# Kernel tuning notes

Hardware: AMD Instinct MI355X
Metric: run time of the kernel (lower is better)

Reference implementation:

```python
import jax, jax.numpy as jnp
import numpy as np

# ---- hash-grid constants (from tcnn Encoding config in __init__) ----
N_LEVELS = 16
F = 2                      # n_features_per_level
LOG2_T = 19
T = 1 << LOG2_T            # hashmap entries per level
BASE_RES = 16
PER_LEVEL_SCALE = 1.447269237440378
PRIMES = np.array([1, 2654435761, 805459861], dtype=np.uint32)
# corner offsets of the unit cube, shape [8, 3]
OFFS = np.stack(np.meshgrid([0, 1], [0, 1], [0, 1], indexing='ij'), -1).reshape(8, 3)


def hash_grid_encode(x01, table):
    """x01: [N,3] in [0,1]; table: [L, T, F]. Returns [N, L*F]."""
    offs = jnp.asarray(OFFS, dtype=jnp.int32)          # [8,3]
    primes = jnp.asarray(PRIMES)                       # [3] uint32
    feats = []
    for l in range(N_LEVELS):
        scale = BASE_RES * (PER_LEVEL_SCALE ** l) - 1.0   # tcnn grid scale
        res = int(np.ceil(scale)) + 1                      # grid resolution
        pos = x01 * scale + 0.5                            # [N,3]
        pos0 = jnp.floor(pos)
        w = pos - pos0                                     # trilinear fracs [N,3]
        pos0 = pos0.astype(jnp.int32)
        corners = jnp.clip(pos0[:, None, :] + offs[None], 0, res - 1)  # [N,8,3]
        if res ** 3 <= T:
            # dense (stride) indexing fits in the table
            idx = (corners[..., 0]
                   + res * corners[..., 1]
                   + res * res * corners[..., 2]).astype(jnp.int32)    # [N,8]
        else:
            # spatial hash with uint32 wraparound multiply + xor
            cu = corners.astype(jnp.uint32)
            idx = ((cu[..., 0] * primes[0])
                   ^ (cu[..., 1] * primes[1])
                   ^ (cu[..., 2] * primes[2])) & jnp.uint32(T - 1)
            idx = idx.astype(jnp.int32)
        # trilinear weights: prod over dims of (w if offset==1 else 1-w)
        wc = jnp.where(offs[None].astype(bool), w[:, None, :], 1.0 - w[:, None, :])
        wc = wc.prod(-1)                                   # [N,8]
        g = table[l][idx]                                  # gather -> [N,8,F]
        feats.append(jnp.einsum('nc,ncf->nf', wc, g))      # [N,F]
    return jnp.concatenate(feats, -1)                      # [N, L*F]


def mlp2(x, w1, w2):
    # 2-layer bias-free MLP with ReLU, matching MLP(num_layers=2, bias=False)
    return jnp.maximum(x @ w1, 0.0) @ w2


def setup_inputs() -> dict:
    key = jax.random.key(0)
    ks = jax.random.split(key, 6)
    N = 1048576
    points = jax.random.uniform(ks[0], (N, 3), jnp.float32, -1.0, 1.0)  # in bbox [-1,1]^3
    # tcnn hash-grid init: uniform(-1e-4, 1e-4)
    hash_table = jax.random.uniform(ks[1], (N_LEVELS, T, F), jnp.float32, -1e-4, 1e-4)
    enc_dim = N_LEVELS * F  # 32
    dw1 = jax.random.normal(ks[2], (enc_dim, 64), jnp.float32) * (1.0 / np.sqrt(enc_dim))
    dw2 = jax.random.normal(ks[3], (64, 1), jnp.float32) * (1.0 / 8.0)
    fw1 = jax.random.normal(ks[4], (enc_dim, 64), jnp.float32) * (1.0 / np.sqrt(enc_dim))
    fw2 = jax.random.normal(ks[5], (64, 3), jnp.float32) * (1.0 / 8.0)
    return {"points": points, "hash_table": hash_table,
            "dw1": dw1, "dw2": dw2, "fw1": fw1, "fw2": fw2}


def reference(points, hash_table, dw1, dw2, fw1, fw2):
    # contract_to_unisphere with bbox [[-1,-1,-1],[1,1,1]] -> [0,1]^3, clamped
    x01 = jnp.clip((points + 1.0) * 0.5, 0.0, 1.0)
    enc = hash_grid_encode(x01, hash_table)               # [N, 32]
    density = jax.nn.softplus(mlp2(enc, dw1, dw2))        # [N, 1]
    color = jax.nn.sigmoid(mlp2(enc, fw1, fw2))           # [N, 3]
    return color, density
```

## Files before the change

### kernel.cpp

```cpp
#include <hip/hip_runtime.h>
#include <hip/hip_bf16.h>
#include <cmath>

#define NLV 16
#define TBL_SIZE (1u << 19)

#define SORT_PPB 8192
#define SORT_THREADS 512
#define SORT_NKEYS 4096

struct LevelConsts {
    float scale[NLV];
    int   res[NLV];
    int   dense[NLV];
};

__device__ __forceinline__ unsigned int f32_to_bf16_rne(float f) {
    unsigned int u = __float_as_uint(f);
    return (u + 0x7FFFu + ((u >> 16) & 1u)) >> 16;
}
__device__ __forceinline__ unsigned int pack_bf16(float a, float b) {
    return f32_to_bf16_rne(a) | (f32_to_bf16_rne(b) << 16);
}
__device__ __forceinline__ short f32_to_bf16_s(float f) {
    return (short)f32_to_bf16_rne(f);
}
__device__ __forceinline__ float bf16lo_to_f32(unsigned int g) {
    return __uint_as_float(g << 16);
}
__device__ __forceinline__ float bf16hi_to_f32(unsigned int g) {
    return __uint_as_float(g & 0xFFFF0000u);
}

typedef __attribute__((ext_vector_type(8))) short bf16x8;
typedef __attribute__((ext_vector_type(4))) float f32x4;
typedef __attribute__((ext_vector_type(2))) unsigned int u32x2;
typedef __attribute__((ext_vector_type(4))) unsigned int u32x4;

__device__ __forceinline__ unsigned spread3(unsigned x) {
    x &= 0x3FFu;
    x = (x | (x << 16)) & 0x030000FFu;
    x = (x | (x << 8))  & 0x0300F00Fu;
    x = (x | (x << 4))  & 0x030C30C3u;
    x = (x | (x << 2))  & 0x09249249u;
    return x;
}
__device__ __forceinline__ unsigned key12(float px, float py, float pz) {
    float x = fminf(fmaxf((px + 1.0f) * 0.5f, 0.0f), 1.0f);
    float y = fminf(fmaxf((py + 1.0f) * 0.5f, 0.0f), 1.0f);
    float z = fminf(fmaxf((pz + 1.0f) * 0.5f, 0.0f), 1.0f);
    int ix = min((int)(x * 16.0f), 15);
    int iy = min((int)(y * 16.0f), 15);
    int iz = min((int)(z * 16.0f), 15);
    return spread3((unsigned)ix) | (spread3((unsigned)iy) << 1) | (spread3((unsigned)iz) << 2);
}

__global__ __launch_bounds__(SORT_THREADS) void cvt_and_sort(
    const float* __restrict__ tablef32, unsigned int* __restrict__ tbl_out, int npairs,
    const float* __restrict__ pts, f32x4* __restrict__ spts4, int N, int sortBlocks)
{
    __shared__ unsigned hist[SORT_NKEYS];
    __shared__ unsigned wsum[SORT_THREADS / 64];

    if ((int)blockIdx.x < sortBlocks) {
        const int sb   = blockIdx.x;
        const int base = sb * SORT_PPB;
        const int cnt  = min(SORT_PPB, N - base);
        const int tid  = threadIdx.x;
        const int lane = tid & 63, wid = tid >> 6;

        for (int i = tid; i < SORT_NKEYS; i += SORT_THREADS) hist[i] = 0u;
        __syncthreads();

        unsigned short keys[16];
#pragma unroll
        for (int q = 0; q < 16; q++) {
            int idx = q * SORT_THREADS + tid;
            unsigned k = 0xFFFFu;
            if (idx < cnt) {
                int p = base + idx;
                float px = pts[3 * p + 0];
                float py = pts[3 * p + 1];
                float pz = pts[3 * p + 2];
                k = key12(px, py, pz);
                atomicAdd(&hist[k], 1u);
            }
            keys[q] = (unsigned short)k;
        }
        __syncthreads();

        unsigned loc[8], s = 0;
#pragma unroll
        for (int j = 0; j < 8; j++) { loc[j] = hist[tid * 8 + j]; s += loc[j]; }
        unsigned x = s;
#pragma unroll
        for (int d = 1; d < 64; d <<= 1) {
            unsigned y = __shfl_up(x, d, 64);
            if (lane >= d) x += y;
        }
        unsigned wex = x - s;
        if (lane == 63) wsum[wid] = x;
        __syncthreads();
        if (tid == 0) {
            unsigned r = 0;
            for (int i = 0; i < SORT_THREADS / 64; i++) { unsigned t = wsum[i]; wsum[i] = r; r += t; }
        }
        __syncthreads();
        unsigned run = wex + wsum[wid];
#pragma unroll
        for (int j = 0; j < 8; j++) { hist[tid * 8 + j] = run; run += loc[j]; }
        __syncthreads();

#pragma unroll
        for (int q = 0; q < 16; q++) {
            int idx = q * SORT_THREADS + tid;
            if (idx < cnt) {
                int p = base + idx;
                float px = pts[3 * p + 0];
                float py = pts[3 * p + 1];
                float pz = pts[3 * p + 2];
                unsigned pos = atomicAdd(&hist[keys[q]], 1u);
                f32x4 o;
                o.x = px; o.y = py; o.z = pz; o.w = __uint_as_float((unsigned)p);
                spts4[base + pos] = o;
            }
        }
    } else {
        int b = blockIdx.x - sortBlocks;
        int n2 = npairs >> 1;
        int i = b * SORT_THREADS + threadIdx.x;
        int stride = ((int)gridDim.x - sortBlocks) * SORT_THREADS;
        const f32x4* in4 = (const f32x4*)tablef32;
        u32x2* out2 = (u32x2*)tbl_out;
        for (; i < n2; i += stride) {
            f32x4 v = __builtin_nontemporal_load(&in4[i]);
            u32x2 o;
            o.x = pack_bf16(v.x, v.y);
            o.y = pack_bf16(v.z, v.w);
            __builtin_nontemporal_store(o, &out2[i]);
        }
    }
}

__global__ __launch_bounds__(256) void cvt_table(const float* __restrict__ in,
                                                 unsigned int* __restrict__ out, int npairs) {
    int n2 = npairs >> 1;
    int i = blockIdx.x * 256 + threadIdx.x;
    int stride = gridDim.x * 256;
    const f32x4* in4 = (const f32x4*)in;
    u32x2* out2 = (u32x2*)out;
    for (; i < n2; i += stride) {
        f32x4 v = __builtin_nontemporal_load(&in4[i]);
        u32x2 o;
        o.x = pack_bf16(v.x, v.y);
        o.y = pack_bf16(v.z, v.w);
        __builtin_nontemporal_store(o, &out2[i]);
    }
}

#define ENC_P 4
template<int PSTRIDE>
__global__ __launch_bounds__(256) void encode_lvl(
    const float* __restrict__ points,
    const unsigned int* __restrict__ tbl,
    unsigned int* __restrict__ enc,
    int N, LevelConsts C)
{
    const int level = blockIdx.y;
    const float sc    = C.scale[level];
    const int   res   = C.res[level];
    const int   dense = C.dense[level];
    const unsigned int* __restrict__ t = tbl + (size_t)level * TBL_SIZE;
    unsigned int* __restrict__ eo = enc + (size_t)level * N;

    const int base = blockIdx.x * (256 * ENC_P) + threadIdx.x;

    int   pt[ENC_P];
    int   valid[ENC_P];
    float wx[ENC_P], wy[ENC_P], wz[ENC_P];
    unsigned int i0a[ENC_P][4], i1a[ENC_P][4];

#pragma unroll
    for (int q = 0; q < ENC_P; q++) {
        pt[q] = base + q * 256;
        valid[q] = pt[q] < N;
        int p = valid[q] ? pt[q] : 0;
        float px, py, pz;
        if (PSTRIDE == 4) {
            f32x4 v = *(const f32x4*)&points[(size_t)p * 4];
            px = v.x; py = v.y; pz = v.z;
        } else {
            px = points[p * 3 + 0];
            py = points[p * 3 + 1];
            pz = points[p * 3 + 2];
        }
        float x = fminf(fmaxf((px + 1.0f) * 0.5f, 0.0f), 1.0f);
        float y = fminf(fmaxf((py + 1.0f) * 0.5f, 0.0f), 1.0f);
        float z = fminf(fmaxf((pz + 1.0f) * 0.5f, 0.0f), 1.0f);

        float fx = x * sc + 0.5f;
        float fy = y * sc + 0.5f;
        float fz = z * sc + 0.5f;
        float f0x = floorf(fx), f0y = floorf(fy), f0z = floorf(fz);
        wx[q] = fx - f0x; wy[q] = fy - f0y; wz[q] = fz - f0z;
        int ix0 = min(max((int)f0x, 0), res - 1);
        int iy0 = min(max((int)f0y, 0), res - 1);
        int iz0 = min(max((int)f0z, 0), res - 1);
        int ix1 = min(ix0 + 1, res - 1);
        int iy1 = min(iy0 + 1, res - 1);
        int iz1 = min(iz0 + 1, res - 1);

#pragma unroll
        for (int m = 0; m < 4; m++) {
            unsigned int uy = (unsigned int)((m & 1) ? iy1 : iy0);
            unsigned int uz = (unsigned int)((m & 2) ? iz1 : iz0);
            unsigned int i0, i1;
            if (dense) {
                unsigned int b = (unsigned int)res * uy + (unsigned int)(res * res) * uz;
                i0 = (unsigned int)ix0 + b;
                i1 = (unsigned int)ix1 + b;
            } else {
                unsigned int H = uy * 2654435761u ^ uz * 805459861u;
                i0 = ((unsigned int)ix0 ^ H) & (TBL_SIZE - 1u);
                i1 = ((unsigned int)ix1 ^ H) & (TBL_SIZE - 1u);
            }
            i0a[q][m] = i0;
            i1a[q][m] = i1;
        }
    }

    u32x2 pr[ENC_P][4];
#pragma unroll
    for (int q = 0; q < ENC_P; q++)
#pragma unroll
        for (int m = 0; m < 4; m++)
            pr[q][m] = *(const u32x2*)(t + (i0a[q][m] & ~1u));

    unsigned int ex[ENC_P][4];
#pragma unroll
    for (int q = 0; q < ENC_P; q++)
#pragma unroll
        for (int m = 0; m < 4; m++) {
            unsigned int i0 = i0a[q][m], i1 = i1a[q][m];
            unsigned int e = 0u;
            if (i1 != (i0 ^ 1u)) e = t[i1];
            ex[q][m] = e;
        }

#pragma unroll
    for (int q = 0; q < ENC_P; q++) {
        float e0 = 0.0f, e1 = 0.0f;
        float wxq = wx[q];
#pragma unroll
        for (int m = 0; m < 4; m++) {
            unsigned int i0 = i0a[q][m], i1 = i1a[q][m];
            u32x2 P = pr[q][m];
            unsigned int v0   = (i0 & 1u) ? P.y : P.x;
            unsigned int vpar = (i0 & 1u) ? P.x : P.y;
            unsigned int v1   = (i1 == (i0 ^ 1u)) ? vpar : ex[q][m];
            float wyz = (((m & 1) ? wy[q] : 1.0f - wy[q])) *
                        (((m & 2) ? wz[q] : 1.0f - wz[q]));
            float w0 = wyz * (1.0f - wxq);
            float w1 = wyz * wxq;
            e0 = fmaf(w0, bf16lo_to_f32(v0), e0);
            e0 = fmaf(w1, bf16lo_to_f32(v1), e0);
            e1 = fmaf(w0, bf16hi_to_f32(v0), e1);
            e1 = fmaf(w1, bf16hi_to_f32(v1), e1);
        }
        if (valid[q]) __builtin_nontemporal_store(pack_bf16(e0, e1), &eo[pt[q]]);
    }
}

__global__ __launch_bounds__(256, 4) void mlp_kernel(
    const unsigned int* __restrict__ enc,
    const float* __restrict__ dw1, const float* __restrict__ dw2,
    const float* __restrict__ fw1, const float* __restrict__ fw2,
    const unsigned int* __restrict__ perm,
    float* __restrict__ out, int N, int ntiles)
{
    __shared__ unsigned int hsh[4][16][68];
    __shared__ float sOut[4][256];

    const int tid  = threadIdx.x;
    const int wave = tid >> 6;
    const int lane = tid & 63;
    const int l15 = lane & 15;
    const int quad = lane >> 4;

    bf16x8 B1[8];
#pragma unroll
    for (int nt = 0; nt < 8; nt++) {
        int col = nt * 16 + l15;
        const float* w = (col < 64) ? (dw1 + col) : (fw1 + (col - 64));
#pragma unroll
        for (int j = 0; j < 8; j++) {
            int k = quad * 8 + j;
            B1[nt][j] = f32_to_bf16_s(w[k * 64]);
        }
    }

    bf16x8 B2[4];
#pragma unroll
    for (int s = 0; s < 4; s++) {
#pragma unroll
        for (int j = 0; j < 8; j++) {
            int k_lds = s * 32 + quad * 8 + j;
            int hu = ((k_lds & 7) << 4) | (k_lds >> 3);
            float v = 0.0f;
            if (l15 == 0)      v = (hu < 64)  ? dw2[hu] : 0.0f;
            else if (l15 < 4)  v = (hu >= 64) ? fw2[(hu - 64) * 3 + (l15 - 1)] : 0.0f;
            B2[s][j] = f32_to_bf16_s(v);
        }
    }

    for (int tile = blockIdx.x; tile < ntiles; tile += gridDim.x) {
        const int wbase = tile * 256 + wave * 64;

        unsigned int au[4][4];
#pragma unroll
        for (int sub = 0; sub < 4; sub++) {
            int ptc = min(wbase + sub * 16 + l15, N - 1);
#pragma unroll
            for (int j = 0; j < 4; j++)
                au[sub][j] = enc[(size_t)(quad * 4 + j) * N + ptc];
        }

#pragma unroll
        for (int sub = 0; sub < 4; sub++) {
            union { unsigned int u[4]; bf16x8 v; } acvt;
#pragma unroll
            for (int j = 0; j < 4; j++) acvt.u[j] = au[sub][j];

            f32x4 acc1[8];
#pragma unroll
            for (int nt = 0; nt < 8; nt++) {
                acc1[nt] = (f32x4){0.0f, 0.0f, 0.0f, 0.0f};
                acc1[nt] = __builtin_amdgcn_mfma_f32_16x16x32_bf16(acvt.v, B1[nt], acc1[nt], 0, 0, 0);
            }

#pragma unroll
            for (int r = 0; r < 4; r++) {
                u32x4 pk;
#pragma unroll
                for (int d = 0; d < 4; d++) {
                    float h0 = fmaxf(acc1[2 * d + 0][r], 0.0f);
                    float h1 = fmaxf(acc1[2 * d + 1][r], 0.0f);
                    pk[d] = pack_bf16(h0, h1);
                }
                *(u32x4*)&hsh[wave][quad * 4 + r][l15 * 4] = pk;
            }

            f32x4 p0 = (f32x4){0,0,0,0}, p1 = (f32x4){0,0,0,0};
            f32x4 p2 = (f32x4){0,0,0,0}, p3 = (f32x4){0,0,0,0};
            {
                bf16x8 a0 = *(const bf16x8*)&hsh[wave][l15][0 * 16 + quad * 4];
                bf16x8 a1 = *(const bf16x8*)&hsh[wave][l15][1 * 16 + quad * 4];
                bf16x8 a2 = *(const bf16x8*)&hsh[wave][l15][2 * 16 + quad * 4];
                bf16x8 a3 = *(const bf16x8*)&hsh[wave][l15][3 * 16 + quad * 4];
                p0 = __builtin_amdgcn_mfma_f32_16x16x32_bf16(a0, B2[0], p0, 0, 0, 0);
                p1 = __builtin_amdgcn_mfma_f32_16x16x32_bf16(a1, B2[1], p1, 0, 0, 0);
                p2 = __builtin_amdgcn_mfma_f32_16x16x32_bf16(a2, B2[2], p2, 0, 0, 0);
                p3 = __builtin_amdgcn_mfma_f32_16x16x32_bf16(a3, B2[3], p3, 0, 0, 0);
            }
            f32x4 acc2;
#pragma unroll
            for (int r = 0; r < 4; r++) acc2[r] = (p0[r] + p1[r]) + (p2[r] + p3[r]);

            if (l15 < 4) {
#pragma unroll
                for (int r = 0; r < 4; r++)
                    sOut[wave][(sub * 16 + quad * 4 + r) * 4 + l15] = acc2[r];
            }
        }

        if (perm) {
            int p = wbase + lane;
            if (p < N) {
                unsigned int o = perm[(size_t)p * 4 + 3];
                f32x4 v = *(const f32x4*)&sOut[wave][lane * 4];
                float d = v[0];
                d = (d > 20.0f) ? d : log1pf(expf(d));
                out[(size_t)3 * N + o] = d;
                float r0 = 1.0f / (1.0f + expf(-v[1]));
                float g0 = 1.0f / (1.0f + expf(-v[2]));
                float b0 = 1.0f / (1.0f + expf(-v[3]));
                out[(size_t)o * 3 + 0] = r0;
                out[(size_t)o * 3 + 1] = g0;
                out[(size_t)o * 3 + 2] = b0;
            }
        } else {
            long long cmax = ((long long)N - wbase) * 3;
#pragma unroll
            for (int round = 0; round < 3; round++) {
                int f = round * 64 + lane;
                int lp = f / 3, c = f - lp * 3;
                float v = sOut[wave][lp * 4 + 1 + c];
                v = 1.0f / (1.0f + expf(-v));
                if (f < cmax) out[(size_t)wbase * 3 + f] = v;
            }
            {
                int p = wbase + lane;
                float v = sOut[wave][lane * 4];
                v = (v > 20.0f) ? v : log1pf(expf(v));
                if (p < N) out[(size_t)3 * N + p] = v;
            }
        }
    }
}

__global__ __launch_bounds__(256) void nerf_fused(
    const float* __restrict__ points,
    const float* __restrict__ table,
    const float* __restrict__ dw1, const float* __restrict__ dw2,
    const float* __restrict__ fw1, const float* __restrict__ fw2,
    float* __restrict__ out, int N, LevelConsts C)
{
    __shared__ float sD[64 * 32];
    __shared__ float sF[64 * 32];
    __shared__ float sDw2[64];
    __shared__ float sFw2[64 * 3];

    for (int idx = threadIdx.x; idx < 2048; idx += 256) {
        int i = idx >> 6;
        int j = idx & 63;
        sD[j * 32 + i] = dw1[idx];
        sF[j * 32 + i] = fw1[idx];
    }
    if (threadIdx.x < 64)  sDw2[threadIdx.x] = dw2[threadIdx.x];
    if (threadIdx.x < 192) sFw2[threadIdx.x] = fw2[threadIdx.x];
    __syncthreads();

    int gid = blockIdx.x * 256 + threadIdx.x;
    if (gid >= N) return;

    float px = points[gid * 3 + 0];
    float py = points[gid * 3 + 1];
    float pz = points[gid * 3 + 2];
    float x = fminf(fmaxf((px + 1.0f) * 0.5f, 0.0f), 1.0f);
    float y = fminf(fmaxf((py + 1.0f) * 0.5f, 0.0f), 1.0f);
    float z = fminf(fmaxf((pz + 1.0f) * 0.5f, 0.0f), 1.0f);

    float enc[32];

#pragma unroll
    for (int l = 0; l < NLV; l++) {
        const float sc = C.scale[l];
        const int   res = C.res[l];
        const int   dense = C.dense[l];
        const float* __restrict__ tbl = table + (size_t)l * TBL_SIZE * 2;

        float fx = x * sc + 0.5f;
        float fy = y * sc + 0.5f;
        float fz = z * sc + 0.5f;
        float f0x = floorf(fx), f0y = floorf(fy), f0z = floorf(fz);
        float wx = fx - f0x, wy = fy - f0y, wz = fz - f0z;
        int ix0 = min(max((int)f0x, 0), res - 1);
        int iy0 = min(max((int)f0y, 0), res - 1);
        int iz0 = min(max((int)f0z, 0), res - 1);
        int ix1 = min(ix0 + 1, res - 1);
        int iy1 = min(iy0 + 1, res - 1);
        int iz1 = min(iz0 + 1, res - 1);

        float e0 = 0.0f, e1 = 0.0f;
#pragma unroll
        for (int c = 0; c < 8; c++) {
            int cx = (c & 4) ? ix1 : ix0;
            int cy = (c & 2) ? iy1 : iy0;
            int cz = (c & 1) ? iz1 : iz0;
            float wgt = (((c & 4) ? wx : 1.0f - wx) *
                         ((c & 2) ? wy : 1.0f - wy)) *
                         ((c & 1) ? wz : 1.0f - wz);
            unsigned int idx;
            if (dense) {
                idx = (unsigned int)(cx + res * cy + res * res * cz);
            } else {
                idx = ((unsigned int)cx * 1u
                     ^ (unsigned int)cy * 2654435761u
                     ^ (unsigned int)cz * 805459861u) & (TBL_SIZE - 1u);
            }
            const float2 g = *(const float2*)(tbl + (size_t)idx * 2);
            e0 = fmaf(wgt, g.x, e0);
            e1 = fmaf(wgt, g.y, e1);
        }
        enc[2 * l + 0] = e0;
        enc[2 * l + 1] = e1;
    }

    float dacc = 0.0f, c0 = 0.0f, c1 = 0.0f, c2 = 0.0f;
    for (int j = 0; j < 64; j++) {
        float hd = 0.0f, hf = 0.0f;
        const float* __restrict__ colD = &sD[j * 32];
        const float* __restrict__ colF = &sF[j * 32];
#pragma unroll
        for (int i = 0; i < 32; i++) {
            hd = fmaf(enc[i], colD[i], hd);
            hf = fmaf(enc[i], colF[i], hf);
        }
        hd = fmaxf(hd, 0.0f);
        hf = fmaxf(hf, 0.0f);
        dacc = fmaf(hd, sDw2[j], dacc);
        c0 = fmaf(hf, sFw2[j * 3 + 0], c0);
        c1 = fmaf(hf, sFw2[j * 3 + 1], c1);
        c2 = fmaf(hf, sFw2[j * 3 + 2], c2);
    }

    float density = (dacc > 20.0f) ? dacc : log1pf(expf(dacc));
    out[gid * 3 + 0] = 1.0f / (1.0f + expf(-c0));
    out[gid * 3 + 1] = 1.0f / (1.0f + expf(-c1));
    out[gid * 3 + 2] = 1.0f / (1.0f + expf(-c2));
    out[(size_t)3 * N + gid] = density;
}

extern "C" void kernel_launch(void* const* d_in, const int* in_sizes, int n_in,
                              void* d_out, int out_size, void* d_ws, size_t ws_size,
                              hipStream_t stream) {
    const float* points = (const float*)d_in[0];
    const float* table  = (const float*)d_in[1];
    const float* dw1    = (const float*)d_in[2];
    const float* dw2    = (const float*)d_in[3];
    const float* fw1    = (const float*)d_in[4];
    const float* fw2    = (const float*)d_in[5];
    int N = in_sizes[0] / 3;

    LevelConsts C;
    for (int l = 0; l < NLV; l++) {
        double s = 16.0 * pow(1.447269237440378, (double)l) - 1.0;
        C.scale[l] = (float)s;
        int res = (int)ceil(s) + 1;
        C.res[l] = res;
        C.dense[l] = ((long long)res * res * res <= (long long)TBL_SIZE) ? 1 : 0;
    }

    auto align256 = [](size_t x) { return (x + 255) & ~(size_t)255; };
    const size_t tbl_bytes  = align256((size_t)NLV * TBL_SIZE * 4);
    const size_t enc_bytes  = align256((size_t)N * NLV * 4);
    const size_t spts_bytes = align256((size_t)N * 4 * 4);

    int ntiles = (N + 255) / 256;
    int chunks = (N + 256 * ENC_P - 1) / (256 * ENC_P);
    int npairs = NLV * TBL_SIZE;

    if (ws_size >= tbl_bytes + enc_bytes + spts_bytes) {
        char* wp = (char*)d_ws;
        unsigned int* tbl_bf16 = (unsigned int*)wp;            wp += tbl_bytes;
        unsigned int* enc_ws   = (unsigned int*)wp;            wp += enc_bytes;
        f32x4*        spts4    = (f32x4*)wp;                   wp += spts_bytes;

        int sortBlocks = (N + SORT_PPB - 1) / SORT_PPB;
        cvt_and_sort<<<sortBlocks + 1024, SORT_THREADS, 0, stream>>>(
            table, tbl_bf16, npairs, points, spts4, N, sortBlocks);

        encode_lvl<4><<<dim3(chunks, NLV), 256, 0, stream>>>((const float*)spts4,
                                                             tbl_bf16, enc_ws, N, C);

        mlp_kernel<<<1792, 256, 0, stream>>>(enc_ws, dw1, dw2, fw1, fw2,
                                             (const unsigned int*)spts4,
                                             (float*)d_out, N, ntiles);
    } else if (ws_size >= tbl_bytes + enc_bytes) {
        unsigned int* tbl_bf16 = (unsigned int*)d_ws;
        unsigned int* enc_ws   = (unsigned int*)((char*)d_ws + tbl_bytes);

        cvt_table<<<1024, 256, 0, stream>>>(table, tbl_bf16, npairs);

        encode_lvl<3><<<dim3(chunks, NLV), 256, 0, stream>>>(points, tbl_bf16, enc_ws, N, C);

        mlp_kernel<<<1792, 256, 0, stream>>>(enc_ws, dw1, dw2, fw1, fw2, nullptr,
                                             (float*)d_out, N, ntiles);
    } else {
        int blocks = (N + 255) / 256;
        nerf_fused<<<blocks, 256, 0, stream>>>(points, table, dw1, dw2, fw1, fw2,
                                               (float*)d_out, N, C);
    }
}
```

Measured before the change: 518.6 us.

## Replace per-block Morton sort with global 15-bit counting sort of points

Points are now sorted globally by a 15-bit Morton key (32^3 cells) through a four-kernel counting sort: per-block histograms packed as 16-bit pairs, a column scan across blocks, a scan of the totals, and a scatter. The old sort only reordered points within 8192-point blocks using a 12-bit key. The aim is better spatial locality of hash-table gathers in the encode kernel across the whole input. In exchange it adds three kernel launches, extra workspace for the per-block histograms, a serial column scan, and a 16-bit count packing that limits each key to 65535 points per block.

```diff
diff --git a/kernel.cpp b/kernel.cpp
--- a/kernel.cpp
+++ b/kernel.cpp
@@ -8,6 +8,10 @@
 #define SORT_PPB 8192
 #define SORT_THREADS 512
 #define SORT_NKEYS 4096
+
+#define KB15 32768
+#define PPB2 16384
+#define GS_THREADS 1024
 
 struct LevelConsts {
     float scale[NLV];
@@ -54,6 +58,127 @@
     int iz = min((int)(z * 16.0f), 15);
     return spread3((unsigned)ix) | (spread3((unsigned)iy) << 1) | (spread3((unsigned)iz) << 2);
 }
+__device__ __forceinline__ unsigned key15(float px, float py, float pz) {
+    float x = fminf(fmaxf((px + 1.0f) * 0.5f, 0.0f), 1.0f);
+    float y = fminf(fmaxf((py + 1.0f) * 0.5f, 0.0f), 1.0f);
+    float z = fminf(fmaxf((pz + 1.0f) * 0.5f, 0.0f), 1.0f);
+    int ix = min((int)(x * 32.0f), 31);
+    int iy = min((int)(y * 32.0f), 31);
+    int iz = min((int)(z * 32.0f), 31);
+    return spread3((unsigned)ix) | (spread3((unsigned)iy) << 1) | (spread3((unsigned)iz) << 2);
+}
+
+__global__ __launch_bounds__(GS_THREADS) void cvt_and_hist(
+    const float* __restrict__ tablef32, unsigned int* __restrict__ tbl_out, int npairs,
+    const float* __restrict__ pts, unsigned int* __restrict__ colpre32,
+    int N, int histBlocks)
+{
+    __shared__ unsigned packed[KB15 / 2];
+    if ((int)blockIdx.x < histBlocks) {
+        const int blk = blockIdx.x, base = blk * PPB2, cnt = min(PPB2, N - base);
+        const int tid = threadIdx.x;
+        for (int i = tid; i < KB15 / 2; i += GS_THREADS) packed[i] = 0u;
+        __syncthreads();
+#pragma unroll
+        for (int q = 0; q < PPB2 / GS_THREADS; q++) {
+            int idx = q * GS_THREADS + tid;
+            if (idx < cnt) {
+                int p = base + idx;
+                unsigned k = key15(pts[3 * p + 0], pts[3 * p + 1], pts[3 * p + 2]);
+                atomicAdd(&packed[k >> 1], (k & 1u) ? 0x10000u : 1u);
+            }
+        }
+        __syncthreads();
+        for (int i = tid; i < KB15 / 2; i += GS_THREADS)
+            colpre32[(size_t)blk * (KB15 / 2) + i] = packed[i];
+    } else {
+        int b = blockIdx.x - histBlocks;
+        int n2 = npairs >> 1;
+        int i = b * GS_THREADS + threadIdx.x;
+        int stride = ((int)gridDim.x - histBlocks) * GS_THREADS;
+        const f32x4* in4 = (const f32x4*)tablef32;
+        u32x2* out2 = (u32x2*)tbl_out;
+        for (; i < n2; i += stride) {
+            f32x4 v = __builtin_nontemporal_load(&in4[i]);
+            u32x2 o;
+            o.x = pack_bf16(v.x, v.y);
+            o.y = pack_bf16(v.z, v.w);
+            __builtin_nontemporal_store(o, &out2[i]);
+        }
+    }
+}
+
+__global__ __launch_bounds__(GS_THREADS) void colscan(
+    unsigned int* __restrict__ colpre32, unsigned int* __restrict__ tot, int nblk)
+{
+    int k2 = blockIdx.x * GS_THREADS + threadIdx.x;
+    unsigned run0 = 0, run1 = 0;
+    for (int b = 0; b < nblk; b++) {
+        size_t off = (size_t)b * (KB15 / 2) + k2;
+        unsigned v = colpre32[off];
+        colpre32[off] = run0 | (run1 << 16);
+        run0 += v & 0xFFFFu;
+        run1 += v >> 16;
+    }
+    tot[2 * k2 + 0] = run0;
+    tot[2 * k2 + 1] = run1;
+}
+
+__global__ __launch_bounds__(GS_THREADS) void scan_tot(unsigned int* __restrict__ tot) {
+    __shared__ unsigned wsum[GS_THREADS / 64];
+    const int t = threadIdx.x, lane = t & 63, wid = t >> 6;
+    unsigned loc[KB15 / GS_THREADS];
+    unsigned s = 0;
+#pragma unroll
+    for (int j = 0; j < KB15 / GS_THREADS; j++) { loc[j] = tot[t * (KB15 / GS_THREADS) + j]; s += loc[j]; }
+    unsigned x = s;
+#pragma unroll
+    for (int d = 1; d < 64; d <<= 1) {
+        unsigned y = __shfl_up(x, d, 64);
+        if (lane >= d) x += y;
+    }
+    unsigned wex = x - s;
+    if (lane == 63) wsum[wid] = x;
+    __syncthreads();
+    if (t == 0) {
+        unsigned r = 0;
+        for (int i = 0; i < GS_THREADS / 64; i++) { unsigned tt = wsum[i]; wsum[i] = r; r += tt; }
+    }
+    __syncthreads();
+    unsigned run = wex + wsum[wid];
+#pragma unroll
+    for (int j = 0; j < KB15 / GS_THREADS; j++) { tot[t * (KB15 / GS_THREADS) + j] = run; run += loc[j]; }
+}
+
+__global__ __launch_bounds__(GS_THREADS) void global_scatter(
+    const float* __restrict__ pts, const unsigned int* __restrict__ colpre32,
+    const unsigned int* __restrict__ tot, f32x4* __restrict__ spts4, int N)
+{
+    __shared__ unsigned packed[KB15 / 2];
+    const int blk = blockIdx.x, base = blk * PPB2, cnt = min(PPB2, N - base);
+    const int tid = threadIdx.x;
+    for (int i = tid; i < KB15 / 2; i += GS_THREADS) packed[i] = 0u;
+    __syncthreads();
+#pragma unroll
+    for (int q = 0; q < PPB2 / GS_THREADS; q++) {
+        int idx = q * GS_THREADS + tid;
+        if (idx < cnt) {
+            int p = base + idx;
+            float px = pts[3 * p + 0];
+            float py = pts[3 * p + 1];
+            float pz = pts[3 * p + 2];
+            unsigned k = key15(px, py, pz);
+            unsigned old = atomicAdd(&packed[k >> 1], (k & 1u) ? 0x10000u : 1u);
+            unsigned rank = (old >> ((k & 1u) * 16)) & 0xFFFFu;
+            unsigned cb = colpre32[(size_t)blk * (KB15 / 2) + (k >> 1)];
+            unsigned colbase = (k & 1u) ? (cb >> 16) : (cb & 0xFFFFu);
+            unsigned pos = tot[k] + colbase + rank;
+            f32x4 o;
+            o.x = px; o.y = py; o.z = pz; o.w = __uint_as_float((unsigned)p);
+            spts4[pos] = o;
+        }
+    }
+}
 
 __global__ __launch_bounds__(SORT_THREADS) void cvt_and_sort(
     const float* __restrict__ tablef32, unsigned int* __restrict__ tbl_out, int npairs,
@@ -79,10 +204,7 @@
             unsigned k = 0xFFFFu;
             if (idx < cnt) {
                 int p = base + idx;
-                float px = pts[3 * p + 0];
-                float py = pts[3 * p + 1];
-                float pz = pts[3 * p + 2];
-                k = key12(px, py, pz);
+                k = key12(pts[3 * p + 0], pts[3 * p + 1], pts[3 * p + 2]);
                 atomicAdd(&hist[k], 1u);
             }
             keys[q] = (unsigned short)k;
@@ -103,7 +225,7 @@
         __syncthreads();
         if (tid == 0) {
             unsigned r = 0;
-            for (int i = 0; i < SORT_THREADS / 64; i++) { unsigned t = wsum[i]; wsum[i] = r; r += t; }
+            for (int i = 0; i < SORT_THREADS / 64; i++) { unsigned t2 = wsum[i]; wsum[i] = r; r += t2; }
         }
         __syncthreads();
         unsigned run = wex + wsum[wid];
@@ -536,15 +658,38 @@
     const size_t enc_bytes  = align256((size_t)N * NLV * 4);
     const size_t spts_bytes = align256((size_t)N * 4 * 4);
 
+    int nblk = (N + PPB2 - 1) / PPB2;
+    const size_t colpre_bytes = align256((size_t)nblk * (KB15 / 2) * 4);
+    const size_t tot_bytes    = align256((size_t)KB15 * 4);
+
     int ntiles = (N + 255) / 256;
     int chunks = (N + 256 * ENC_P - 1) / (256 * ENC_P);
     int npairs = NLV * TBL_SIZE;
 
-    if (ws_size >= tbl_bytes + enc_bytes + spts_bytes) {
+    if (ws_size >= tbl_bytes + enc_bytes + spts_bytes + colpre_bytes + tot_bytes) {
         char* wp = (char*)d_ws;
         unsigned int* tbl_bf16 = (unsigned int*)wp;            wp += tbl_bytes;
         unsigned int* enc_ws   = (unsigned int*)wp;            wp += enc_bytes;
         f32x4*        spts4    = (f32x4*)wp;                   wp += spts_bytes;
+        unsigned int* colpre   = (unsigned int*)wp;            wp += colpre_bytes;
+        unsigned int* tot      = (unsigned int*)wp;            wp += tot_bytes;
+
+        cvt_and_hist<<<nblk + 512, GS_THREADS, 0, stream>>>(
+            table, tbl_bf16, npairs, points, colpre, N, nblk);
+        colscan<<<KB15 / 2 / GS_THREADS, GS_THREADS, 0, stream>>>(colpre, tot, nblk);
+        scan_tot<<<1, GS_THREADS, 0, stream>>>(tot);
+        global_scatter<<<nblk, GS_THREADS, 0, stream>>>(points, colpre, tot, spts4, N);
+
+        encode_lvl<4><<<dim3(chunks, NLV), 256, 0, stream>>>((const float*)spts4,
+                                                             tbl_bf16, enc_ws, N, C);
+        mlp_kernel<<<1792, 256, 0, stream>>>(enc_ws, dw1, dw2, fw1, fw2,
+                                             (const unsigned int*)spts4,
+                                             (float*)d_out, N, ntiles);
+    } else if (ws_size >= tbl_bytes + enc_bytes + spts_bytes) {
+        char* wp = (char*)d_ws;
+        unsigned int* tbl_bf16 = (unsigned int*)wp;            wp += tbl_bytes;
+        unsigned int* enc_ws   = (unsigned int*)wp;            wp += enc_bytes;
+        f32x4*        spts4    = (f32x4*)wp;                   wp += spts_bytes;
 
         int sortBlocks = (N + SORT_PPB - 1) / SORT_PPB;
         cvt_and_sort<<<sortBlocks + 1024, SORT_THREADS, 0, stream>>>(
@@ -552,7 +697,6 @@
 
         encode_lvl<4><<<dim3(chunks, NLV), 256, 0, stream>>>((const float*)spts4,
                                                              tbl_bf16, enc_ws, N, C);
-
         mlp_kernel<<<1792, 256, 0, stream>>>(enc_ws, dw1, dw2, fw1, fw2,
                                              (const unsigned int*)spts4,
                                              (float*)d_out, N, ntiles);
@@ -561,9 +705,7 @@
         unsigned int* enc_ws   = (unsigned int*)((char*)d_ws + tbl_bytes);
 
         cvt_table<<<1024, 256, 0, stream>>>(table, tbl_bf16, npairs);
-
         encode_lvl<3><<<dim3(chunks, NLV), 256, 0, stream>>>(points, tbl_bf16, enc_ws, N, C);
-
         mlp_kernel<<<1792, 256, 0, stream>>>(enc_ws, dw1, dw2, fw1, fw2, nullptr,
                                              (float*)d_out, N, ntiles);
     } else {
```

After: 515.9 us. No clear change (-0.5%).

## Replace per-block local sort with global 15-bit Morton counting sort

Applied to the files above, without the earlier changes.

Points were previously sorted only within 8192-point blocks by a 12-bit Morton key. They are now sorted globally with a 32768-bin histogram built by global atomics, a single-block scan, and an atomic scatter. The goal is better spatial locality of hash-table gathers in the encode kernel. The cost is two extra kernel launches plus a memset, heavy global atomic contention, and a scatter whose order within each bin is nondeterministic.

```diff
diff --git a/kernel.cpp b/kernel.cpp
--- a/kernel.cpp
+++ b/kernel.cpp
@@ -8,6 +8,9 @@
 #define SORT_PPB 8192
 #define SORT_THREADS 512
 #define SORT_NKEYS 4096
+
+#define KB15 32768
+#define SCAN_THREADS 1024
 
 struct LevelConsts {
     float scale[NLV];
@@ -54,6 +57,87 @@
     int iz = min((int)(z * 16.0f), 15);
     return spread3((unsigned)ix) | (spread3((unsigned)iy) << 1) | (spread3((unsigned)iz) << 2);
 }
+__device__ __forceinline__ unsigned key15(float px, float py, float pz) {
+    float x = fminf(fmaxf((px + 1.0f) * 0.5f, 0.0f), 1.0f);
+    float y = fminf(fmaxf((py + 1.0f) * 0.5f, 0.0f), 1.0f);
+    float z = fminf(fmaxf((pz + 1.0f) * 0.5f, 0.0f), 1.0f);
+    int ix = min((int)(x * 32.0f), 31);
+    int iy = min((int)(y * 32.0f), 31);
+    int iz = min((int)(z * 32.0f), 31);
+    return spread3((unsigned)ix) | (spread3((unsigned)iy) << 1) | (spread3((unsigned)iz) << 2);
+}
+
+__global__ __launch_bounds__(256) void cvt_and_hist_at(
+    const float* __restrict__ tablef32, unsigned int* __restrict__ tbl_out, int npairs,
+    const float* __restrict__ pts, unsigned int* __restrict__ hist, int N, int histBlocks)
+{
+    if ((int)blockIdx.x < histBlocks) {
+        int i = blockIdx.x * 256 + threadIdx.x;
+        int stride = histBlocks * 256;
+        for (; i < N; i += stride) {
+            unsigned k = key15(pts[3 * i + 0], pts[3 * i + 1], pts[3 * i + 2]);
+            atomicAdd(&hist[k], 1u);
+        }
+    } else {
+        int b = blockIdx.x - histBlocks;
+        int n2 = npairs >> 1;
+        int i = b * 256 + threadIdx.x;
+        int stride = ((int)gridDim.x - histBlocks) * 256;
+        const f32x4* in4 = (const f32x4*)tablef32;
+        u32x2* out2 = (u32x2*)tbl_out;
+        for (; i < n2; i += stride) {
+            f32x4 v = __builtin_nontemporal_load(&in4[i]);
+            u32x2 o;
+            o.x = pack_bf16(v.x, v.y);
+            o.y = pack_bf16(v.z, v.w);
+            __builtin_nontemporal_store(o, &out2[i]);
+        }
+    }
+}
+
+__global__ __launch_bounds__(SCAN_THREADS) void scan_tot(unsigned int* __restrict__ tot) {
+    __shared__ unsigned wsum[SCAN_THREADS / 64];
+    const int t = threadIdx.x, lane = t & 63, wid = t >> 6;
+    unsigned loc[KB15 / SCAN_THREADS];
+    unsigned s = 0;
+#pragma unroll
+    for (int j = 0; j < KB15 / SCAN_THREADS; j++) { loc[j] = tot[t * (KB15 / SCAN_THREADS) + j]; s += loc[j]; }
+    unsigned x = s;
+#pragma unroll
+    for (int d = 1; d < 64; d <<= 1) {
+        unsigned y = __shfl_up(x, d, 64);
+        if (lane >= d) x += y;
+    }
+    unsigned wex = x - s;
+    if (lane == 63) wsum[wid] = x;
+    __syncthreads();
+    if (t == 0) {
+        unsigned r = 0;
+        for (int i = 0; i < SCAN_THREADS / 64; i++) { unsigned tt = wsum[i]; wsum[i] = r; r += tt; }
+    }
+    __syncthreads();
+    unsigned run = wex + wsum[wid];
+#pragma unroll
+    for (int j = 0; j < KB15 / SCAN_THREADS; j++) { tot[t * (KB15 / SCAN_THREADS) + j] = run; run += loc[j]; }
+}
+
+__global__ __launch_bounds__(256) void scatter_at(
+    const float* __restrict__ pts, unsigned int* __restrict__ cur,
+    f32x4* __restrict__ spts4, int N)
+{
+    int i = blockIdx.x * 256 + threadIdx.x;
+    int stride = gridDim.x * 256;
+    for (; i < N; i += stride) {
+        float px = pts[3 * i + 0];
+        float py = pts[3 * i + 1];
+        float pz = pts[3 * i + 2];
+        unsigned k = key15(px, py, pz);
+        unsigned pos = atomicAdd(&cur[k], 1u);
+        f32x4 o;
+        o.x = px; o.y = py; o.z = pz; o.w = __uint_as_float((unsigned)i);
+        spts4[pos] = o;
+    }
+}
 
 __global__ __launch_bounds__(SORT_THREADS) void cvt_and_sort(
     const float* __restrict__ tablef32, unsigned int* __restrict__ tbl_out, int npairs,
@@ -79,10 +163,7 @@
             unsigned k = 0xFFFFu;
             if (idx < cnt) {
                 int p = base + idx;
-                float px = pts[3 * p + 0];
-                float py = pts[3 * p + 1];
-                float pz = pts[3 * p + 2];
-                k = key12(px, py, pz);
+                k = key12(pts[3 * p + 0], pts[3 * p + 1], pts[3 * p + 2]);
                 atomicAdd(&hist[k], 1u);
             }
             keys[q] = (unsigned short)k;
@@ -103,7 +184,7 @@
         __syncthreads();
         if (tid == 0) {
             unsigned r = 0;
-            for (int i = 0; i < SORT_THREADS / 64; i++) { unsigned t = wsum[i]; wsum[i] = r; r += t; }
+            for (int i = 0; i < SORT_THREADS / 64; i++) { unsigned t2 = wsum[i]; wsum[i] = r; r += t2; }
         }
         __syncthreads();
         unsigned run = wex + wsum[wid];
@@ -535,16 +616,35 @@
     const size_t tbl_bytes  = align256((size_t)NLV * TBL_SIZE * 4);
     const size_t enc_bytes  = align256((size_t)N * NLV * 4);
     const size_t spts_bytes = align256((size_t)N * 4 * 4);
+    const size_t hist_bytes = align256((size_t)KB15 * 4);
 
     int ntiles = (N + 255) / 256;
     int chunks = (N + 256 * ENC_P - 1) / (256 * ENC_P);
     int npairs = NLV * TBL_SIZE;
 
-    if (ws_size >= tbl_bytes + enc_bytes + spts_bytes) {
+    if (ws_size >= tbl_bytes + enc_bytes + spts_bytes && enc_bytes >= hist_bytes) {
         char* wp = (char*)d_ws;
         unsigned int* tbl_bf16 = (unsigned int*)wp;            wp += tbl_bytes;
         unsigned int* enc_ws   = (unsigned int*)wp;            wp += enc_bytes;
         f32x4*        spts4    = (f32x4*)wp;                   wp += spts_bytes;
+        unsigned int* hist     = enc_ws;
+
+        hipMemsetAsync(hist, 0, (size_t)KB15 * 4, stream);
+        cvt_and_hist_at<<<2048, 256, 0, stream>>>(table, tbl_bf16, npairs,
+                                                  points, hist, N, 1024);
+        scan_tot<<<1, SCAN_THREADS, 0, stream>>>(hist);
+        scatter_at<<<1024, 256, 0, stream>>>(points, hist, spts4, N);
+
+        encode_lvl<4><<<dim3(chunks, NLV), 256, 0, stream>>>((const float*)spts4,
+                                                             tbl_bf16, enc_ws, N, C);
+        mlp_kernel<<<1792, 256, 0, stream>>>(enc_ws, dw1, dw2, fw1, fw2,
+                                             (const unsigned int*)spts4,
+                                             (float*)d_out, N, ntiles);
+    } else if (ws_size >= tbl_bytes + enc_bytes + spts_bytes) {
+        char* wp = (char*)d_ws;
+        unsigned int* tbl_bf16 = (unsigned int*)wp;            wp += tbl_bytes;
+        unsigned int* enc_ws   = (unsigned int*)wp;            wp += enc_bytes;
+        f32x4*        spts4    = (f32x4*)wp;                   wp += spts_bytes;
 
         int sortBlocks = (N + SORT_PPB - 1) / SORT_PPB;
         cvt_and_sort<<<sortBlocks + 1024, SORT_THREADS, 0, stream>>>(
@@ -552,7 +652,6 @@
 
         encode_lvl<4><<<dim3(chunks, NLV), 256, 0, stream>>>((const float*)spts4,
                                                              tbl_bf16, enc_ws, N, C);
-
         mlp_kernel<<<1792, 256, 0, stream>>>(enc_ws, dw1, dw2, fw1, fw2,
                                              (const unsigned int*)spts4,
                                              (float*)d_out, N, ntiles);
@@ -561,9 +660,7 @@
         unsigned int* enc_ws   = (unsigned int*)((char*)d_ws + tbl_bytes);
 
         cvt_table<<<1024, 256, 0, stream>>>(table, tbl_bf16, npairs);
-
         encode_lvl<3><<<dim3(chunks, NLV), 256, 0, stream>>>(points, tbl_bf16, enc_ws, N, C);
-
         mlp_kernel<<<1792, 256, 0, stream>>>(enc_ws, dw1, dw2, fw1, fw2, nullptr,
                                              (float*)d_out, N, ntiles);
     } else {
```

Result: slower. 563.3 us (+8.6%).
